# Optimization experiments

Hardware: AMD Instinct MI355X
Metric: run time of the kernel (lower is better)

## Reference

```python
import math
import jax, jax.numpy as jnp
import numpy as np

NUM_HEADS = 16
HIDDEN = 1024
HEAD_SIZE = HIDDEN // NUM_HEADS
B, S = 4, 2048


def setup_inputs() -> dict:
    key = jax.random.key(0)
    k1, k2, k3 = jax.random.split(key, 3)
    scale = 1.0 / math.sqrt(HIDDEN)
    return {
        "hidden_states": jax.random.normal(k1, (B, S, HIDDEN), dtype=jnp.float32),
        "attention_mask": jnp.ones((B, S), dtype=jnp.float32),
        "Wq": jax.random.normal(k2, (HIDDEN, HIDDEN), dtype=jnp.float32) * scale,
        "bq": jnp.zeros((HIDDEN,), dtype=jnp.float32),
        "Wk": jax.random.normal(k3, (HIDDEN, HIDDEN), dtype=jnp.float32) * scale,
        "bk": jnp.zeros((HIDDEN,), dtype=jnp.float32),
    }


def reference(hidden_states, attention_mask, Wq, bq, Wk, bk):
    b, s, _ = hidden_states.shape
    # Linear projections (torch Linear: x @ W.T + b)
    q = hidden_states @ Wq.T + bq  # [B,S,H]
    k = hidden_states @ Wk.T + bk  # [B,S,H]
    # split heads: [B, nH, S, dH]
    q = q.reshape(b, s, NUM_HEADS, HEAD_SIZE).transpose(0, 2, 1, 3)
    k = k.reshape(b, s, NUM_HEADS, HEAD_SIZE).transpose(0, 2, 1, 3)
    scores = jnp.einsum("bhqd,bhkd->bhqk", q, k)  # [B,nH,S,S]
    scores = scores / math.sqrt(HEAD_SIZE)  # sqrtatt=True
    scores = jnp.mean(scores, axis=1)  # aggregation='mean' -> [B,S,S]
    scores = scores * attention_mask[:, None, :]  # mask keys (cols)
    scores = scores * attention_mask[:, :, None]  # mask queries (rows)
    return scores
```

## Files before the change

### kernel.cpp

```cpp
#include <hip/hip_runtime.h>
#include <hip/hip_bf16.h>
#include <stdint.h>

#define S_LEN 2048
#define BATCH 4
#define HID 1024
#define M_ROWS (BATCH * S_LEN)

typedef __attribute__((ext_vector_type(8))) short short8;
typedef __attribute__((ext_vector_type(4))) float f32x4;

__device__ __forceinline__ void gload_lds16(const void* g, void* l) {
  __builtin_amdgcn_global_load_lds(
      (const __attribute__((address_space(1))) unsigned int*)g,
      (__attribute__((address_space(3))) unsigned int*)l, 16, 0, 0);
}

template <int N>
__device__ __forceinline__ void wait_vm() {
  if constexpr (N == 0)
    asm volatile("s_waitcnt vmcnt(0)" ::: "memory");
  else
    asm volatile("s_waitcnt vmcnt(4)" ::: "memory");
}

#define CFENCE asm volatile("" ::: "memory")
#define BAR_PRE do { CFENCE; __builtin_amdgcn_s_barrier();                    \
    asm volatile("s_waitcnt lgkmcnt(0)" ::: "memory"); } while (0)
#define BAR_POST do { CFENCE; __builtin_amdgcn_s_barrier(); CFENCE; } while (0)

__global__ __launch_bounds__(256) void convert_all(
    const float* __restrict__ hs, const float* __restrict__ wq,
    const float* __restrict__ wk,
    __hip_bfloat16* __restrict__ hs_bf, __hip_bfloat16* __restrict__ wq_bf,
    __hip_bfloat16* __restrict__ wk_bf) {
  const int NH = M_ROWS * HID;
  const int NW = HID * HID;
  int idx = (blockIdx.x * blockDim.x + threadIdx.x) * 4;
  const float* src;
  __hip_bfloat16* dst;
  int off;
  if (idx < NH)           { src = hs; dst = hs_bf; off = idx; }
  else if (idx < NH + NW) { src = wq; dst = wq_bf; off = idx - NH; }
  else                    { src = wk; dst = wk_bf; off = idx - NH - NW; }
  float4 v = *reinterpret_cast<const float4*>(src + off);
  __hip_bfloat16 tmp[4];
  tmp[0] = __float2bfloat16(v.x);
  tmp[1] = __float2bfloat16(v.y);
  tmp[2] = __float2bfloat16(v.z);
  tmp[3] = __float2bfloat16(v.w);
  *reinterpret_cast<ushort4*>(dst + off) = *reinterpret_cast<const ushort4*>(tmp);
}

template <int NT>
__device__ __forceinline__ void gemm_core_bf(
    const __hip_bfloat16* __restrict__ A, const __hip_bfloat16* __restrict__ B,
    const int lda, const int ldb, __hip_bfloat16* lds, f32x4 acc[8][4]) {
  const int t = threadIdx.x;
  const int wid = t >> 6;
  const int l = t & 63;
  const int lr = l & 15;
  const int lk = l >> 4;
  const int wr = wid >> 2;
  const int wc = wid & 3;
  const int trow = t >> 3;
  const int tslot = (t & 7) ^ (trow & 7);
  const int rsx = lr & 7;

  __hip_bfloat16* const A0 = lds;
  __hip_bfloat16* const A1 = lds + 16384;
  __hip_bfloat16* const B0 = lds + 32768;
  __hip_bfloat16* const B1 = lds + 49152;

  short8 fa[4][2], fb[4][2];

#define STAGE_U(lb, gb, ld, half, kt) do {                                    \
    gload_lds16((gb) + (size_t)((half)*128 + 0  + trow) * (ld) + (kt)*64 +    \
                    tslot * 8,                                                \
                (lb) + ((half)*128 + 0) * 64 + wid * 512);                    \
    gload_lds16((gb) + (size_t)((half)*128 + 64 + trow) * (ld) + (kt)*64 +    \
                    tslot * 8,                                                \
                (lb) + ((half)*128 + 64) * 64 + wid * 512);                   \
  } while (0)

#define LDA_H(mh, Ac) do {                                                    \
    _Pragma("unroll") for (int m = 0; m < 4; ++m)                             \
    _Pragma("unroll") for (int kk = 0; kk < 2; ++kk)                          \
      fa[m][kk] = *reinterpret_cast<const short8*>(                           \
          (Ac) + (wr * 128 + (mh)*64 + m * 16 + lr) * 64 +                    \
          (((kk * 4 + lk) ^ rsx) * 8));                                       \
  } while (0)

#define LDB_H(nh, Bc) do {                                                    \
    _Pragma("unroll") for (int n = 0; n < 2; ++n)                             \
    _Pragma("unroll") for (int kk = 0; kk < 2; ++kk)                          \
      fb[(nh)*2 + n][kk] = *reinterpret_cast<const short8*>(                  \
          (Bc) + (wc * 64 + (nh)*32 + n * 16 + lr) * 64 +                     \
          (((kk * 4 + lk) ^ rsx) * 8));                                       \
  } while (0)

#define MFMA_Q(mh, nh) do {                                                   \
    __builtin_amdgcn_s_setprio(1);                                            \
    _Pragma("unroll") for (int m = 0; m < 4; ++m)                             \
    _Pragma("unroll") for (int n = 0; n < 2; ++n)                             \
    _Pragma("unroll") for (int kk = 0; kk < 2; ++kk)                          \
      acc[(mh)*4 + m][(nh)*2 + n] = __builtin_amdgcn_mfma_f32_16x16x32_bf16(  \
          fb[(nh)*2 + n][kk], fa[m][kk], acc[(mh)*4 + m][(nh)*2 + n],         \
          0, 0, 0);                                                           \
    __builtin_amdgcn_s_setprio(0);                                            \
  } while (0)

  STAGE_U(A0, A, lda, 0, 0); STAGE_U(A0, A, lda, 1, 0);
  STAGE_U(B0, B, ldb, 0, 0); STAGE_U(B0, B, ldb, 1, 0);
  STAGE_U(B1, B, ldb, 0, 1); STAGE_U(B1, B, ldb, 1, 1);
  wait_vm<4>();
  __builtin_amdgcn_s_barrier();
  CFENCE;

#pragma unroll 2
  for (int tt = 0; tt < NT; ++tt) {
    const int cur = tt & 1;
    __hip_bfloat16* const Ac = cur ? A1 : A0;
    __hip_bfloat16* const An = cur ? A0 : A1;
    __hip_bfloat16* const Bc = cur ? B1 : B0;
    LDA_H(0, Ac); LDB_H(0, Bc);
    if (tt + 1 < NT) STAGE_U(An, A, lda, 0, tt + 1);
    BAR_PRE; MFMA_Q(0, 0); BAR_POST;
    LDB_H(1, Bc);
    if (tt + 1 < NT) STAGE_U(An, A, lda, 1, tt + 1);
    BAR_PRE; MFMA_Q(0, 1); BAR_POST;
    LDA_H(1, Ac);
    if (tt + 2 < NT) STAGE_U(Bc, B, ldb, 0, tt + 2);
    BAR_PRE; MFMA_Q(1, 1); BAR_POST;
    if (tt + 2 < NT) STAGE_U(Bc, B, ldb, 1, tt + 2);
    BAR_PRE; MFMA_Q(1, 0);
    if (tt + 2 < NT) wait_vm<4>(); else wait_vm<0>();
    BAR_POST;
  }
#undef STAGE_U
#undef LDA_H
#undef LDB_H
#undef MFMA_Q
}

__global__ __launch_bounds__(512, 2) void proj_gemm(
    const __hip_bfloat16* __restrict__ X,
    const __hip_bfloat16* __restrict__ Wq, const float* __restrict__ bq,
    const __hip_bfloat16* __restrict__ Wk, const float* __restrict__ bk,
    __hip_bfloat16* __restrict__ Qo, __hip_bfloat16* __restrict__ Ko) {
  extern __shared__ char smem[];
  __hip_bfloat16* lds = reinterpret_cast<__hip_bfloat16*>(smem);
  const int bid = blockIdx.x;
  const int xcd = bid & 7, s = bid >> 3;
  const int bm = xcd * 4 + (s & 3);
  const int bn8 = s >> 2;
  const int z = bn8 >> 2;
  const int bn = bn8 & 3;

  const __hip_bfloat16* W = z ? Wk : Wq;
  const float* bias = z ? bk : bq;
  __hip_bfloat16* Out = z ? Ko : Qo;

  f32x4 acc[8][4];
#pragma unroll
  for (int m = 0; m < 8; ++m)
#pragma unroll
    for (int n = 0; n < 4; ++n) acc[m][n] = (f32x4){0.f, 0.f, 0.f, 0.f};

  gemm_core_bf<HID / 64>(X + (size_t)bm * 256 * HID,
                         W + (size_t)bn * 256 * HID, HID, HID, lds, acc);

  const int t = threadIdx.x, wid = t >> 6, l = t & 63;
  const int wr = wid >> 2, wc = wid & 3;
  const int lr = l & 15, lg = l >> 4;
#pragma unroll
  for (int m = 0; m < 8; ++m) {
    const int row = bm * 256 + wr * 128 + m * 16 + lr;
#pragma unroll
    for (int n = 0; n < 4; ++n) {
      const int col0 = bn * 256 + wc * 64 + n * 16 + lg * 4;
      float4 bb = *reinterpret_cast<const float4*>(&bias[col0]);
      f32x4 a = acc[m][n];
      __hip_bfloat16 tmp[4] = {
          __float2bfloat16(a[0] + bb.x), __float2bfloat16(a[1] + bb.y),
          __float2bfloat16(a[2] + bb.z), __float2bfloat16(a[3] + bb.w)};
      *reinterpret_cast<ushort4*>(&Out[(size_t)row * HID + col0]) =
          *reinterpret_cast<const ushort4*>(tmp);
    }
  }
}

__global__ __launch_bounds__(512, 2) void scores_gemm(
    const __hip_bfloat16* __restrict__ Q, const __hip_bfloat16* __restrict__ Km,
    const float* __restrict__ mask, float* __restrict__ out) {
  extern __shared__ char smem[];
  __hip_bfloat16* lds = reinterpret_cast<__hip_bfloat16*>(smem);
  const int bid = blockIdx.x;
  const int xcd = bid & 7, slot = bid >> 3;
  const int b = slot >> 3, sub = slot & 7;
  const int bm = (xcd & 3) * 2 + (sub >> 2);
  const int bn = (xcd >> 2) * 4 + (sub & 3);

  f32x4 acc[8][4];
#pragma unroll
  for (int m = 0; m < 8; ++m)
#pragma unroll
    for (int n = 0; n < 4; ++n) acc[m][n] = (f32x4){0.f, 0.f, 0.f, 0.f};

  gemm_core_bf<HID / 64>(Q + ((size_t)b * S_LEN + bm * 256) * HID,
                         Km + ((size_t)b * S_LEN + bn * 256) * HID, HID, HID,
                         lds, acc);

  const int t = threadIdx.x, wid = t >> 6, l = t & 63;
  const int wr = wid >> 2, wc = wid & 3;
  const int lr = l & 15, lg = l >> 4;
  const float inv = 1.0f / 128.0f;
#pragma unroll
  for (int m = 0; m < 8; ++m) {
    const int row = bm * 256 + wr * 128 + m * 16 + lr;
    const float mr = mask[b * S_LEN + row] * inv;
#pragma unroll
    for (int n = 0; n < 4; ++n) {
      const int col0 = bn * 256 + wc * 64 + n * 16 + lg * 4;
      float4 mcv = *reinterpret_cast<const float4*>(&mask[b * S_LEN + col0]);
      f32x4 a = acc[m][n];
      f32x4 o = {a[0] * mr * mcv.x, a[1] * mr * mcv.y,
                 a[2] * mr * mcv.z, a[3] * mr * mcv.w};
      __builtin_nontemporal_store(
          o, reinterpret_cast<f32x4*>(
                 &out[(size_t)b * S_LEN * S_LEN + (size_t)row * S_LEN + col0]));
    }
  }
}

extern "C" void kernel_launch(void* const* d_in, const int* in_sizes, int n_in,
                              void* d_out, int out_size, void* d_ws,
                              size_t ws_size, hipStream_t stream) {
  const float* hs   = (const float*)d_in[0];
  const float* mask = (const float*)d_in[1];
  const float* Wq   = (const float*)d_in[2];
  const float* bq   = (const float*)d_in[3];
  const float* Wk   = (const float*)d_in[4];
  const float* bk   = (const float*)d_in[5];
  float* out = (float*)d_out;

  char* ws = (char*)d_ws;
  __hip_bfloat16* hs_bf = (__hip_bfloat16*)(ws);
  __hip_bfloat16* wq_bf = (__hip_bfloat16*)(ws + 16777216);
  __hip_bfloat16* wk_bf = (__hip_bfloat16*)(ws + 18874368);
  __hip_bfloat16* q_bf  = (__hip_bfloat16*)(ws + 20971520);
  __hip_bfloat16* k_bf  = (__hip_bfloat16*)(ws + 37748736);

  (void)hipFuncSetAttribute((const void*)proj_gemm,
                            hipFuncAttributeMaxDynamicSharedMemorySize, 131072);
  (void)hipFuncSetAttribute((const void*)scores_gemm,
                            hipFuncAttributeMaxDynamicSharedMemorySize, 131072);

  hipLaunchKernelGGL(convert_all, dim3(10240), dim3(256), 0, stream,
                     hs, Wq, Wk, hs_bf, wq_bf, wk_bf);
  hipLaunchKernelGGL(proj_gemm, dim3(256), dim3(512), 131072, stream,
                     hs_bf, wq_bf, bq, wk_bf, bk, q_bf, k_bf);
  hipLaunchKernelGGL(scores_gemm, dim3(256), dim3(512), 131072, stream,
                     q_bf, k_bf, mask, out);
}
```

Before: 96.50 us.

## Shrink scores GEMM tiles to 128x128 with a custom pipelined 4-wave loop

```diff
diff --git a/kernel.cpp b/kernel.cpp
--- a/kernel.cpp
+++ b/kernel.cpp
@@ -190,45 +190,128 @@
   }
 }
 
-__global__ __launch_bounds__(512, 2) void scores_gemm(
+__global__ __launch_bounds__(256, 2) void scores_gemm(
     const __hip_bfloat16* __restrict__ Q, const __hip_bfloat16* __restrict__ Km,
     const float* __restrict__ mask, float* __restrict__ out) {
   extern __shared__ char smem[];
   __hip_bfloat16* lds = reinterpret_cast<__hip_bfloat16*>(smem);
   const int bid = blockIdx.x;
   const int xcd = bid & 7, slot = bid >> 3;
-  const int b = slot >> 3, sub = slot & 7;
-  const int bm = (xcd & 3) * 2 + (sub >> 2);
-  const int bn = (xcd >> 2) * 4 + (sub & 3);
-
-  f32x4 acc[8][4];
-#pragma unroll
-  for (int m = 0; m < 8; ++m)
+  const int b = slot >> 5, sub = slot & 31;
+  const int bm = (xcd & 3) * 4 + (sub >> 3);
+  const int bn = (xcd >> 2) * 8 + (sub & 7);
+
+  const __hip_bfloat16* A = Q + ((size_t)b * S_LEN + bm * 128) * HID;
+  const __hip_bfloat16* B = Km + ((size_t)b * S_LEN + bn * 128) * HID;
+
+  const int t = threadIdx.x;
+  const int wid = t >> 6;
+  const int l = t & 63;
+  const int lr = l & 15;
+  const int lk = l >> 4;
+  const int wr = wid >> 1;
+  const int wc = wid & 1;
+  const int trow = t >> 3;
+  const int tslot = (t & 7) ^ (trow & 7);
+  const int rsx = lr & 7;
+
+  __hip_bfloat16* const A0 = lds;
+  __hip_bfloat16* const A1 = lds + 8192;
+  __hip_bfloat16* const B0 = lds + 16384;
+  __hip_bfloat16* const B1 = lds + 24576;
+
+  f32x4 acc[4][4];
+#pragma unroll
+  for (int m = 0; m < 4; ++m)
 #pragma unroll
     for (int n = 0; n < 4; ++n) acc[m][n] = (f32x4){0.f, 0.f, 0.f, 0.f};
 
-  gemm_core_bf<HID / 64>(Q + ((size_t)b * S_LEN + bm * 256) * HID,
-                         Km + ((size_t)b * S_LEN + bn * 256) * HID, HID, HID,
-                         lds, acc);
-
-  const int t = threadIdx.x, wid = t >> 6, l = t & 63;
-  const int wr = wid >> 2, wc = wid & 3;
-  const int lr = l & 15, lg = l >> 4;
+  short8 fa[2][2], fb[4][2];
+
+#define STAGE_S(lb, gb, half, kt) do {                                        \
+    gload_lds16((gb) + (size_t)((half)*64 + 0  + trow) * HID + (kt)*64 +      \
+                    tslot * 8,                                                \
+                (lb) + (half)*4096 + wid * 512);                              \
+    gload_lds16((gb) + (size_t)((half)*64 + 32 + trow) * HID + (kt)*64 +      \
+                    tslot * 8,                                                \
+                (lb) + (half)*4096 + 2048 + wid * 512);                       \
+  } while (0)
+
+#define LDA_S(mh, Ac) do {                                                    \
+    _Pragma("unroll") for (int m = 0; m < 2; ++m)                             \
+    _Pragma("unroll") for (int kk = 0; kk < 2; ++kk)                          \
+      fa[m][kk] = *reinterpret_cast<const short8*>(                           \
+          (Ac) + (wr * 64 + (mh)*32 + m * 16 + lr) * 64 +                     \
+          (((kk * 4 + lk) ^ rsx) * 8));                                       \
+  } while (0)
+
+#define LDB_S(nh, Bc) do {                                                    \
+    _Pragma("unroll") for (int n = 0; n < 2; ++n)                             \
+    _Pragma("unroll") for (int kk = 0; kk < 2; ++kk)                          \
+      fb[(nh)*2 + n][kk] = *reinterpret_cast<const short8*>(                  \
+          (Bc) + (wc * 64 + (nh)*32 + n * 16 + lr) * 64 +                     \
+          (((kk * 4 + lk) ^ rsx) * 8));                                       \
+  } while (0)
+
+#define MFMA_S(mh, nh) do {                                                   \
+    __builtin_amdgcn_s_setprio(1);                                            \
+    _Pragma("unroll") for (int m = 0; m < 2; ++m)                             \
+    _Pragma("unroll") for (int n = 0; n < 2; ++n)                             \
+    _Pragma("unroll") for (int kk = 0; kk < 2; ++kk)                          \
+      acc[(mh)*2 + m][(nh)*2 + n] = __builtin_amdgcn_mfma_f32_16x16x32_bf16(  \
+          fb[(nh)*2 + n][kk], fa[m][kk], acc[(mh)*2 + m][(nh)*2 + n],         \
+          0, 0, 0);                                                           \
+    __builtin_amdgcn_s_setprio(0);                                            \
+  } while (0)
+
+  constexpr int NT = HID / 64;
+  STAGE_S(A0, A, 0, 0); STAGE_S(A0, A, 1, 0);
+  STAGE_S(B0, B, 0, 0); STAGE_S(B0, B, 1, 0);
+  STAGE_S(B1, B, 0, 1); STAGE_S(B1, B, 1, 1);
+  wait_vm<4>();
+  __builtin_amdgcn_s_barrier();
+  CFENCE;
+
+#pragma unroll 2
+  for (int tt = 0; tt < NT; ++tt) {
+    const int cur = tt & 1;
+    __hip_bfloat16* const Ac = cur ? A1 : A0;
+    __hip_bfloat16* const An = cur ? A0 : A1;
+    __hip_bfloat16* const Bc = cur ? B1 : B0;
+    LDA_S(0, Ac); LDB_S(0, Bc);
+    if (tt + 1 < NT) STAGE_S(An, A, 0, tt + 1);
+    BAR_PRE; MFMA_S(0, 0); BAR_POST;
+    LDB_S(1, Bc);
+    if (tt + 1 < NT) STAGE_S(An, A, 1, tt + 1);
+    BAR_PRE; MFMA_S(0, 1); BAR_POST;
+    LDA_S(1, Ac);
+    if (tt + 2 < NT) STAGE_S(Bc, B, 0, tt + 2);
+    BAR_PRE; MFMA_S(1, 1); BAR_POST;
+    if (tt + 2 < NT) STAGE_S(Bc, B, 1, tt + 2);
+    BAR_PRE; MFMA_S(1, 0);
+    if (tt + 2 < NT) wait_vm<4>(); else wait_vm<0>();
+    BAR_POST;
+  }
+#undef STAGE_S
+#undef LDA_S
+#undef LDB_S
+#undef MFMA_S
+
+  const int lg = l >> 4;
   const float inv = 1.0f / 128.0f;
 #pragma unroll
-  for (int m = 0; m < 8; ++m) {
-    const int row = bm * 256 + wr * 128 + m * 16 + lr;
+  for (int m = 0; m < 4; ++m) {
+    const int row = bm * 128 + wr * 64 + m * 16 + lr;
     const float mr = mask[b * S_LEN + row] * inv;
 #pragma unroll
     for (int n = 0; n < 4; ++n) {
-      const int col0 = bn * 256 + wc * 64 + n * 16 + lg * 4;
+      const int col0 = bn * 128 + wc * 64 + n * 16 + lg * 4;
       float4 mcv = *reinterpret_cast<const float4*>(&mask[b * S_LEN + col0]);
       f32x4 a = acc[m][n];
-      f32x4 o = {a[0] * mr * mcv.x, a[1] * mr * mcv.y,
-                 a[2] * mr * mcv.z, a[3] * mr * mcv.w};
-      __builtin_nontemporal_store(
-          o, reinterpret_cast<f32x4*>(
-                 &out[(size_t)b * S_LEN * S_LEN + (size_t)row * S_LEN + col0]));
+      float4 o = {a[0] * mr * mcv.x, a[1] * mr * mcv.y,
+                  a[2] * mr * mcv.z, a[3] * mr * mcv.w};
+      *reinterpret_cast<float4*>(
+          &out[(size_t)b * S_LEN * S_LEN + (size_t)row * S_LEN + col0]) = o;
     }
   }
 }
@@ -254,12 +337,12 @@
   (void)hipFuncSetAttribute((const void*)proj_gemm,
                             hipFuncAttributeMaxDynamicSharedMemorySize, 131072);
   (void)hipFuncSetAttribute((const void*)scores_gemm,
-                            hipFuncAttributeMaxDynamicSharedMemorySize, 131072);
+                            hipFuncAttributeMaxDynamicSharedMemorySize, 65536);
 
   hipLaunchKernelGGL(convert_all, dim3(10240), dim3(256), 0, stream,
                      hs, Wq, Wk, hs_bf, wq_bf, wk_bf);
   hipLaunchKernelGGL(proj_gemm, dim3(256), dim3(512), 131072, stream,
                      hs_bf, wq_bf, bq, wk_bf, bk, q_bf, k_bf);
-  hipLaunchKernelGGL(scores_gemm, dim3(256), dim3(512), 131072, stream,
+  hipLaunchKernelGGL(scores_gemm, dim3(1024), dim3(256), 65536, stream,
                      q_bf, k_bf, mask, out);
 }
```

Result: slower. 98.63 us (+2.2%).
